# Optimization experiments

Hardware: AMD Instinct MI355X
Metric: run time of the kernel (lower is better)

The kernel has to match this reference:

```python
import jax, jax.numpy as jnp
import numpy as np
from jax import lax

P = 8  # patch_size

def _conv(x, w, b, pad):
    y = lax.conv_general_dilated(x, w, (1, 1), [(pad, pad), (pad, pad)],
                                 dimension_numbers=('NCHW', 'OIHW', 'NCHW'))
    return y + b[None, :, None, None]

def _unfold(t):
    # t: [B,1,H,W] -> [B, L, P*P], matching torch.nn.Unfold(kernel=P, stride=P)
    B, _, H, W = t.shape
    t = t.reshape(B, H // P, P, W // P, P)
    t = t.transpose(0, 1, 3, 2, 4)
    return t.reshape(B, (H // P) * (W // P), P * P)

def setup_inputs() -> dict:
    key = jax.random.key(0)
    ks = jax.random.split(key, 10)
    d = {}
    d['x'] = jax.random.normal(ks[0], (4, 3, 512, 512), dtype=jnp.float32)
    d['fea'] = jax.random.normal(ks[1], (4, 64, 512, 512), dtype=jnp.float32)
    # conv_img: Conv2d(3,64,7x7,pad3) then Conv2d(64,1,3x3,pad1)
    d['w_img1'] = jax.random.normal(ks[2], (64, 3, 7, 7), dtype=jnp.float32) * 0.05
    d['b_img1'] = jax.random.normal(ks[3], (64,), dtype=jnp.float32) * 0.05
    d['w_img2'] = jax.random.normal(ks[4], (1, 64, 3, 3), dtype=jnp.float32) * 0.05
    d['b_img2'] = jax.random.normal(ks[5], (1,), dtype=jnp.float32) * 0.05
    # conv_feamap: Conv2d(64,1,1x1)
    d['w_fea'] = jax.random.normal(ks[6], (1, 64, 1, 1), dtype=jnp.float32) * 0.05
    d['b_fea'] = jax.random.normal(ks[7], (1,), dtype=jnp.float32) * 0.05
    # resolution_trans: Linear(P*P, 2*P*P, bias=False), Linear(2*P*P, P*P, bias=False), ReLU
    d['w1'] = jax.random.normal(ks[8], (2 * P * P, P * P), dtype=jnp.float32) * 0.1
    d['w2'] = jax.random.normal(ks[9], (P * P, 2 * P * P), dtype=jnp.float32) * 0.1
    return d

def reference(x, fea, w_img1, b_img1, w_img2, b_img2, w_fea, b_fea, w1, w2):
    ATT_DEPTH_SCALE = 4.0  # 2**att_depth * 2**att_depth with att_depth=1
    ini_img = _conv(_conv(x, w_img1, b_img1, 3), w_img2, b_img2, 1)      # [B,1,H,W]
    feamap = _conv(fea, w_fea, b_fea, 0) / ATT_DEPTH_SCALE               # [B,1,H,W]
    trans = lambda u: jax.nn.relu((u @ w1.T) @ w2.T)                     # [B,L,P*P]
    u_img = trans(_unfold(ini_img))
    u_fea = trans(_unfold(feamap))
    att = jnp.einsum('blp,bmp->blm', u_img, u_fea) / (P * P)             # [B,L,L]
    return att[:, None]                                                  # [B,1,L,L]
```

## Files before the change

### kernel.cpp

```cpp
#include <hip/hip_runtime.h>

#define IMG  262144
#define NPAT 4096

#define OFF_C9   0
#define OFF_W    256
#define OFF_G    4352
#define OFF_INI  5696
#define OFF_FMAP (OFF_INI + 4*IMG)
#define OFF_V    (OFF_FMAP + 4*IMG)

typedef short v8s __attribute__((ext_vector_type(8)));
typedef float v4f __attribute__((ext_vector_type(4)));

__device__ inline unsigned short f2bf(float x) {
  unsigned u = __float_as_uint(x);
  u = u + 0x7FFF + ((u >> 16) & 1);
  return (unsigned short)(u >> 16);
}
__device__ inline float bf2f(unsigned short h) {
  return __uint_as_float(((unsigned)h) << 16);
}

__global__ __launch_bounds__(256) void k_prep(
    const float* __restrict__ fea,   const float* __restrict__ wfea,
    const float* __restrict__ bfea,
    const float* __restrict__ w1img, const float* __restrict__ b1img,
    const float* __restrict__ w2img, const float* __restrict__ b2img,
    const float* __restrict__ w1,    const float* __restrict__ w2,
    float* __restrict__ ws) {
  int bid = blockIdx.x, tid = threadIdx.x;
  if (bid < 1024) {
    int pix = bid * 1024 + tid * 4;
    int b = pix >> 18;
    int rem = pix & (IMG - 1);
    const float* src = fea + (size_t)(b * 64) * IMG + rem;
    v4f acc = {0.f, 0.f, 0.f, 0.f};
    #pragma unroll 8
    for (int c = 0; c < 64; ++c) {
      float w = wfea[c];
      v4f v = __builtin_nontemporal_load((const v4f*)(src + (size_t)c * IMG));
      acc += w * v;
    }
    float bb = bfea[0];
    acc = (acc + bb) * 0.25f;
    *(v4f*)(ws + OFF_FMAP + pix) = acc;
    return;
  }
  if (bid < 1040) {
    int j = (bid - 1024) * 4 + (tid >> 6), q = tid & 63;
    float acc = 0.f;
    for (int k = 0; k < 128; ++k) acc += w2[j * 128 + k] * w1[k * 64 + q];
    ws[OFF_W + q * 64 + j] = acc;
    return;
  }
  if (bid == 1040) {
    if (tid < 243) {
      int i = tid / 81, r = tid % 81, dy = r / 9, dx = r % 9;
      float acc = 0.f;
      for (int m = 0; m < 64; ++m)
        for (int ky = 0; ky < 3; ++ky) {
          int k1y = dy - ky; if (k1y < 0 || k1y > 6) continue;
          for (int kx = 0; kx < 3; ++kx) {
            int k1x = dx - kx; if (k1x < 0 || k1x > 6) continue;
            acc += w2img[m * 9 + ky * 3 + kx] * w1img[(m * 3 + i) * 49 + k1y * 7 + k1x];
          }
        }
      ws[OFF_C9 + tid] = acc;
    } else if (tid == 243) {
      float acc = b2img[0];
      for (int m = 0; m < 64; ++m) {
        float s = 0.f;
        for (int k = 0; k < 9; ++k) s += w2img[m * 9 + k];
        acc += b1img[m] * s;
      }
      ws[OFF_C9 + 243] = acc;
    }
    return;
  }
  int gidx = (bid - 1041) * 256 + tid;
  if (gidx < 1323) {
    int k2 = gidx / 147, t = gidx % 147;
    float acc = 0.f;
    for (int m = 0; m < 64; ++m) acc += w2img[m * 9 + k2] * w1img[m * 147 + t];
    ws[OFF_G + gidx] = acc;
  } else if (gidx < 1332) {
    int k2 = gidx - 1323;
    float acc = 0.f;
    for (int m = 0; m < 64; ++m) acc += w2img[m * 9 + k2] * b1img[m];
    ws[OFF_G + gidx] = acc;
  }
}

__global__ __launch_bounds__(256) void k_conv9(const float* __restrict__ x,
                                               const float* __restrict__ ws,
                                               float* __restrict__ ini) {
  __shared__ float sIn[3][24][72];
  int bid = blockIdx.x, tid = threadIdx.x;
  int b = bid >> 8, t = bid & 255;
  int ty0 = (t >> 3) << 4, tx0 = (t & 7) << 6;
  for (int idx = tid; idx < 3 * 24 * 72; idx += 256) {
    int c = idx / 1728, r = (idx % 1728) / 72, cc = idx % 72;
    int gy = ty0 + r - 4, gx = tx0 + cc - 4;
    float v = 0.f;
    if ((unsigned)gy < 512u && (unsigned)gx < 512u)
      v = x[(b * 3 + c) * IMG + gy * 512 + gx];
    sIn[c][r][cc] = v;
  }
  __syncthreads();
  const float* Cw = ws + OFF_C9;
  int ty = tid >> 4, tx = (tid & 15) << 2;
  float bc = Cw[243];
  float a0 = bc, a1 = bc, a2 = bc, a3 = bc;
  #pragma unroll
  for (int i = 0; i < 3; ++i)
    #pragma unroll
    for (int dy = 0; dy < 9; ++dy) {
      const float* rowp = &sIn[i][ty + dy][tx];
      float4 r0 = *(const float4*)rowp;
      float4 r1 = *(const float4*)(rowp + 4);
      float4 r2 = *(const float4*)(rowp + 8);
      float tt[12] = {r0.x, r0.y, r0.z, r0.w, r1.x, r1.y, r1.z, r1.w,
                      r2.x, r2.y, r2.z, r2.w};
      #pragma unroll
      for (int dx = 0; dx < 9; ++dx) {
        float w = Cw[i * 81 + dy * 9 + dx];
        a0 += w * tt[dx];     a1 += w * tt[dx + 1];
        a2 += w * tt[dx + 2]; a3 += w * tt[dx + 3];
      }
    }
  float4 o = {a0, a1, a2, a3};
  *(float4*)&ini[b * IMG + (ty0 + ty) * 512 + tx0 + tx] = o;
}

__global__ __launch_bounds__(256) void k_ring(const float* __restrict__ x,
                                              const float* __restrict__ ws,
                                              float* __restrict__ ini) {
  int gid = blockIdx.x * 256 + threadIdx.x;
  if (gid >= 4 * 2044) return;
  int b = gid / 2044;
  int r = gid % 2044;
  int py, px;
  if (r < 512)       { py = 0;            px = r;        }
  else if (r < 1024) { py = 511;          px = r - 512;  }
  else if (r < 1534) { py = r - 1024 + 1; px = 0;        }
  else               { py = r - 1534 + 1; px = 511;      }
  const float* G  = ws + OFF_G;
  const float* Gb = G + 1323;
  const float* xb = x + (size_t)(b * 3) * IMG;
  float corr = 0.f;
  for (int k2y = 0; k2y < 3; ++k2y) {
    int qy = py + k2y - 1;
    for (int k2x = 0; k2x < 3; ++k2x) {
      int qx = px + k2x - 1;
      if (!((unsigned)qy >= 512u || (unsigned)qx >= 512u)) continue;
      int k2 = k2y * 3 + k2x;
      float acc = Gb[k2];
      for (int i = 0; i < 3; ++i)
        for (int k1y = 0; k1y < 7; ++k1y) {
          int xy = qy + k1y - 3;
          if ((unsigned)xy >= 512u) continue;
          const float* xrow = xb + i * IMG + xy * 512;
          const float* Grow = G + k2 * 147 + i * 49 + k1y * 7;
          for (int k1x = 0; k1x < 7; ++k1x) {
            int xx = qx + k1x - 3;
            if ((unsigned)xx >= 512u) continue;
            acc += Grow[k1x] * xrow[xx];
          }
        }
      corr += acc;
    }
  }
  ini[b * IMG + py * 512 + px] -= corr;
}

__global__ __launch_bounds__(256) void k_trans(float* __restrict__ ws) {
  __shared__ float Us[64][68];
  int bid = blockIdx.x, tid = threadIdx.x;
  int s = bid >> 8, b = (bid >> 6) & 3, py = bid & 63;
  const float* src = ws + (s ? OFF_FMAP : OFF_INI) + b * IMG + py * 8 * 512;
  unsigned short* Vh = (unsigned short*)(ws + OFF_V) + (s ? 2097152 : 0) + b * NPAT * 64;
  unsigned short* Vl = Vh + 1048576;
  #pragma unroll
  for (int i = 0; i < 4; ++i) {
    int idx = tid + 256 * i;
    int row = idx >> 7;
    int c4  = (idx & 127) * 4;
    float4 v = *(const float4*)(src + row * 512 + c4);
    int px = c4 >> 3, c = c4 & 7;
    *(float4*)&Us[px][row * 8 + c] = v;
  }
  int j = tid & 63, wid = tid >> 6;
  float wc[64];
  #pragma unroll
  for (int q = 0; q < 64; ++q) wc[q] = ws[OFF_W + q * 64 + j];
  __syncthreads();
  #pragma unroll
  for (int i = 0; i < 16; ++i) {
    int lp = wid * 16 + i;
    float acc = 0.f;
    #pragma unroll
    for (int q4 = 0; q4 < 16; ++q4) {
      float4 u = *(const float4*)&Us[lp][q4 * 4];
      acc += u.x * wc[4*q4] + u.y * wc[4*q4+1] + u.z * wc[4*q4+2] + u.w * wc[4*q4+3];
    }
    acc = fmaxf(acc, 0.f);
    unsigned short h = f2bf(acc);
    unsigned short lo = f2bf(acc - bf2f(h));
    int lg = py * 64 + lp;
    Vh[lg * 64 + j] = h;
    Vl[lg * 64 + j] = lo;
  }
}

__global__ __launch_bounds__(256) void k_att(const float* __restrict__ ws,
                                             float* __restrict__ out) {
  __shared__ unsigned short lds[4][128][64];
  int bid0 = blockIdx.x;
  int bid = (bid0 & 7) * 512 + (bid0 >> 3);
  int tid = threadIdx.x;
  int b = bid >> 10, t = bid & 1023;
  int l0 = (t >> 5) << 7, m0 = (t & 31) << 7;
  const unsigned short* V = (const unsigned short*)(ws + OFF_V);
  const unsigned short* pA_h = V + (b * NPAT + l0) * 64;
  const unsigned short* pA_l = V + 1048576 + (b * NPAT + l0) * 64;
  const unsigned short* pB_h = V + 2097152 + (b * NPAT + m0) * 64;
  const unsigned short* pB_l = V + 3145728 + (b * NPAT + m0) * 64;
  #pragma unroll
  for (int i = 0; i < 4; ++i) {
    int idx = tid + 256 * i;
    int row = idx >> 3, sg = idx & 7;
    int p = (sg ^ (row & 7)) * 8;
    *(uint4*)&lds[0][row][p] = *(const uint4*)(pA_h + row * 64 + sg * 8);
    *(uint4*)&lds[1][row][p] = *(const uint4*)(pA_l + row * 64 + sg * 8);
    *(uint4*)&lds[2][row][p] = *(const uint4*)(pB_h + row * 64 + sg * 8);
    *(uint4*)&lds[3][row][p] = *(const uint4*)(pB_l + row * 64 + sg * 8);
  }
  __syncthreads();
  int lane = tid & 63, wid = tid >> 6;
  int wm = (wid & 1) << 6, wn = (wid >> 1) << 6;
  int mlo = lane & 15, quad = lane >> 4;
  v4f acc[4][4] = {};
  #pragma unroll
  for (int kh = 0; kh < 2; ++kh) {
    int sL = quad + 4 * kh;
    v8s ah[4], al[4], bh[4], bl[4];
    #pragma unroll
    for (int mi = 0; mi < 4; ++mi) {
      int r = wm + mi * 16 + mlo;
      int p = (sL ^ (r & 7)) * 8;
      ah[mi] = *(const v8s*)&lds[0][r][p];
      al[mi] = *(const v8s*)&lds[1][r][p];
    }
    #pragma unroll
    for (int ni = 0; ni < 4; ++ni) {
      int r = wn + ni * 16 + mlo;
      int p = (sL ^ (r & 7)) * 8;
      bh[ni] = *(const v8s*)&lds[2][r][p];
      bl[ni] = *(const v8s*)&lds[3][r][p];
    }
    #pragma unroll
    for (int mi = 0; mi < 4; ++mi)
      #pragma unroll
      for (int ni = 0; ni < 4; ++ni) {
        acc[mi][ni] = __builtin_amdgcn_mfma_f32_16x16x32_bf16(ah[mi], bh[ni], acc[mi][ni], 0, 0, 0);
        acc[mi][ni] = __builtin_amdgcn_mfma_f32_16x16x32_bf16(ah[mi], bl[ni], acc[mi][ni], 0, 0, 0);
        acc[mi][ni] = __builtin_amdgcn_mfma_f32_16x16x32_bf16(al[mi], bh[ni], acc[mi][ni], 0, 0, 0);
      }
  }
  float* o = out + (size_t)b * 16777216;
  #pragma unroll
  for (int mi = 0; mi < 4; ++mi)
    #pragma unroll
    for (int ni = 0; ni < 4; ++ni) {
      int col = m0 + wn + ni * 16 + mlo;
      #pragma unroll
      for (int rr = 0; rr < 4; ++rr) {
        int row = l0 + wm + mi * 16 + quad * 4 + rr;
        __builtin_nontemporal_store(acc[mi][ni][rr] * 0.015625f,
                                    o + (size_t)row * 4096 + col);
      }
    }
}

extern "C" void kernel_launch(void* const* d_in, const int* in_sizes, int n_in,
                              void* d_out, int out_size, void* d_ws, size_t ws_size,
                              hipStream_t stream) {
  const float* x      = (const float*)d_in[0];
  const float* fea    = (const float*)d_in[1];
  const float* w_img1 = (const float*)d_in[2];
  const float* b_img1 = (const float*)d_in[3];
  const float* w_img2 = (const float*)d_in[4];
  const float* b_img2 = (const float*)d_in[5];
  const float* w_fea  = (const float*)d_in[6];
  const float* b_fea  = (const float*)d_in[7];
  const float* w1     = (const float*)d_in[8];
  const float* w2     = (const float*)d_in[9];
  float* ws  = (float*)d_ws;
  float* out = (float*)d_out;

  k_prep  <<<1047, 256, 0, stream>>>(fea, w_fea, b_fea, w_img1, b_img1,
                                     w_img2, b_img2, w1, w2, ws);
  k_conv9 <<<1024, 256, 0, stream>>>(x, ws, ws + OFF_INI);
  k_ring  <<<32,   256, 0, stream>>>(x, ws, ws + OFF_INI);
  k_trans <<<512,  256, 0, stream>>>(ws);
  k_att   <<<4096, 256, 0, stream>>>(ws, out);
}
```

Measured before the change: 591.8 us.

## Stage attention output tile through LDS for coalesced vector stores; widen fea reduction

The attention kernel now writes its 128x128 accumulator tile into shared memory, reusing the operand buffer with a padded stride, and then each thread issues contiguous 16-byte nontemporal stores of full rows. Before, each lane wrote scattered 4-byte elements. This targets write efficiency on the 256 MB output, which dominates traffic, at the cost of two extra barriers and a larger LDS footprint (about 67 KB) that may lower occupancy. Separately, the 1x1 fea conv now handles 8 pixels per thread with regular loads instead of nontemporal ones, which halves that kernel's block count.

New measurement: 606.0 us. 1.02x slower.

```diff
diff --git a/kernel.cpp b/kernel.cpp
--- a/kernel.cpp
+++ b/kernel.cpp
@@ -30,31 +30,35 @@
     const float* __restrict__ w1,    const float* __restrict__ w2,
     float* __restrict__ ws) {
   int bid = blockIdx.x, tid = threadIdx.x;
-  if (bid < 1024) {
-    int pix = bid * 1024 + tid * 4;
+  if (bid < 512) {
+    int pix = bid * 2048 + tid * 8;
     int b = pix >> 18;
     int rem = pix & (IMG - 1);
     const float* src = fea + (size_t)(b * 64) * IMG + rem;
-    v4f acc = {0.f, 0.f, 0.f, 0.f};
+    v4f a0 = {0.f, 0.f, 0.f, 0.f}, a1 = {0.f, 0.f, 0.f, 0.f};
     #pragma unroll 8
     for (int c = 0; c < 64; ++c) {
       float w = wfea[c];
-      v4f v = __builtin_nontemporal_load((const v4f*)(src + (size_t)c * IMG));
-      acc += w * v;
+      v4f v0 = *(const v4f*)(src + (size_t)c * IMG);
+      v4f v1 = *(const v4f*)(src + (size_t)c * IMG + 4);
+      a0 += w * v0;
+      a1 += w * v1;
     }
     float bb = bfea[0];
-    acc = (acc + bb) * 0.25f;
-    *(v4f*)(ws + OFF_FMAP + pix) = acc;
+    a0 = (a0 + bb) * 0.25f;
+    a1 = (a1 + bb) * 0.25f;
+    *(v4f*)(ws + OFF_FMAP + pix)     = a0;
+    *(v4f*)(ws + OFF_FMAP + pix + 4) = a1;
     return;
   }
-  if (bid < 1040) {
-    int j = (bid - 1024) * 4 + (tid >> 6), q = tid & 63;
+  if (bid < 528) {
+    int j = (bid - 512) * 4 + (tid >> 6), q = tid & 63;
     float acc = 0.f;
     for (int k = 0; k < 128; ++k) acc += w2[j * 128 + k] * w1[k * 64 + q];
     ws[OFF_W + q * 64 + j] = acc;
     return;
   }
-  if (bid == 1040) {
+  if (bid == 528) {
     if (tid < 243) {
       int i = tid / 81, r = tid % 81, dy = r / 9, dx = r % 9;
       float acc = 0.f;
@@ -78,7 +82,7 @@
     }
     return;
   }
-  int gidx = (bid - 1041) * 256 + tid;
+  int gidx = (bid - 529) * 256 + tid;
   if (gidx < 1323) {
     int k2 = gidx / 147, t = gidx % 147;
     float acc = 0.f;
@@ -215,7 +219,10 @@
 
 __global__ __launch_bounds__(256) void k_att(const float* __restrict__ ws,
                                              float* __restrict__ out) {
-  __shared__ unsigned short lds[4][128][64];
+  __shared__ __align__(16) unsigned char smem[128 * 132 * 4];
+  unsigned short (*lds)[128][64] = (unsigned short(*)[128][64])smem;
+  float (*Cs)[132] = (float(*)[132])smem;
+
   int bid0 = blockIdx.x;
   int bid = (bid0 & 7) * 512 + (bid0 >> 3);
   int tid = threadIdx.x;
@@ -268,19 +275,27 @@
         acc[mi][ni] = __builtin_amdgcn_mfma_f32_16x16x32_bf16(al[mi], bh[ni], acc[mi][ni], 0, 0, 0);
       }
   }
-  float* o = out + (size_t)b * 16777216;
+  __syncthreads();
   #pragma unroll
   for (int mi = 0; mi < 4; ++mi)
     #pragma unroll
     for (int ni = 0; ni < 4; ++ni) {
-      int col = m0 + wn + ni * 16 + mlo;
+      int col = wn + ni * 16 + mlo;
       #pragma unroll
       for (int rr = 0; rr < 4; ++rr) {
-        int row = l0 + wm + mi * 16 + quad * 4 + rr;
-        __builtin_nontemporal_store(acc[mi][ni][rr] * 0.015625f,
-                                    o + (size_t)row * 4096 + col);
+        int row = wm + mi * 16 + quad * 4 + rr;
+        Cs[row][col] = acc[mi][ni][rr] * 0.015625f;
       }
     }
+  __syncthreads();
+  float* o = out + (size_t)b * 16777216 + (size_t)l0 * 4096 + m0;
+  #pragma unroll
+  for (int r = 0; r < 16; ++r) {
+    int row = r * 8 + (tid >> 5);
+    int col = (tid & 31) * 4;
+    v4f val = *(const v4f*)&Cs[row][col];
+    __builtin_nontemporal_store(val, (v4f*)(o + (size_t)row * 4096 + col));
+  }
 }
 
 extern "C" void kernel_launch(void* const* d_in, const int* in_sizes, int n_in,
@@ -299,7 +314,7 @@
   float* ws  = (float*)d_ws;
   float* out = (float*)d_out;
 
-  k_prep  <<<1047, 256, 0, stream>>>(fea, w_fea, b_fea, w_img1, b_img1,
+  k_prep  <<<535,  256, 0, stream>>>(fea, w_fea, b_fea, w_img1, b_img1,
                                      w_img2, b_img2, w1, w2, ws);
   k_conv9 <<<1024, 256, 0, stream>>>(x, ws, ws + OFF_INI);
   k_ring  <<<32,   256, 0, stream>>>(x, ws, ws + OFF_INI);
```
